# Kernel tuning notes

Hardware: AMD Instinct MI355X
Metric: run time of the kernel (lower is better)

## Reference

```python
import jax, jax.numpy as jnp
import numpy as np

N = 50000      # nodes per graph
E = 1600000    # edges per graph
D_IN = 128
D_HID = 128
D_OUT = 128
D_GF = 128
N_LAYERS = 3   # input->hid, hid->hid (hidden_layer=1), hid->out


def setup_inputs() -> dict:
    key = jax.random.key(0)
    ks = jax.random.split(key, 24)
    inp = {
        "feat_p": jax.random.normal(ks[0], (N, D_IN), jnp.float32),
        "src_p": jax.random.randint(ks[1], (E,), 0, N, jnp.int32),
        "dst_p": jax.random.randint(ks[2], (E,), 0, N, jnp.int32),
        "feat_s": jax.random.normal(ks[3], (N, D_IN), jnp.float32),
        "src_s": jax.random.randint(ks[4], (E,), 0, N, jnp.int32),
        "dst_s": jax.random.randint(ks[5], (E,), 0, N, jnp.int32),
    }
    dims = [(D_IN, D_HID), (D_HID, D_HID), (D_HID, D_OUT)]
    for i, (di, do) in enumerate(dims):
        inp[f"W{i}"] = jax.random.normal(ks[6 + 2 * i], (di, do), jnp.float32) * 0.05
        inp[f"b{i}"] = jnp.zeros((do,), jnp.float32)
    inp["Wr"] = jax.random.normal(ks[14], (D_OUT, D_GF), jnp.float32) * 0.05
    inp["br"] = jnp.zeros((D_GF,), jnp.float32)
    inp["Wm1"] = jax.random.normal(ks[15], (2 * D_GF, D_GF), jnp.float32) * 0.05
    inp["bm1"] = jnp.zeros((D_GF,), jnp.float32)
    inp["Wm2"] = jax.random.normal(ks[16], (D_GF, 1), jnp.float32) * 0.05
    inp["bm2"] = jnp.zeros((1,), jnp.float32)
    return inp


def _gcn_stack(feat, src, dst, layers):
    """Stacked GCN: mean over incoming messages, then linear.
    NOTE: the original SingleGCN never applies its ReLU (bug preserved)."""
    n = feat.shape[0]
    deg = jax.ops.segment_sum(jnp.ones_like(src, feat.dtype), dst, num_segments=n)
    inv_deg = (1.0 / jnp.maximum(deg, 1.0))[:, None]  # [N,1]
    h = feat
    for W, b in layers:
        msg = h[src]                                           # [E,d] gather
        agg = jax.ops.segment_sum(msg, dst, num_segments=n)    # [N,d] scatter-add
        h = (agg * inv_deg) @ W + b                            # mean + linear
    return h


def reference(feat_p, src_p, dst_p, feat_s, src_s, dst_s,
              W0, b0, W1, b1, W2, b2, Wr, br, Wm1, bm1, Wm2, bm2):
    layers = [(W0, b0), (W1, b1), (W2, b2)]
    h_p = _gcn_stack(feat_p, src_p, dst_p, layers)
    h_s = _gcn_stack(feat_s, src_s, dst_s, layers)
    # ReadOut: mean over nodes -> linear -> sigmoid
    g_p = jax.nn.sigmoid(jnp.mean(h_p, axis=0) @ Wr + br)  # [D_GF]
    g_s = jax.nn.sigmoid(jnp.mean(h_s, axis=0) @ Wr + br)
    # Match: concat -> linear -> linear -> sigmoid
    c = jnp.concatenate([g_p, g_s], axis=-1)               # [2*D_GF]
    d = (c @ Wm1 + bm1) @ Wm2 + bm2                        # [1]
    return jax.nn.sigmoid(d)
```

## Files before the change

### kernel.cpp

```cpp
#include <hip/hip_runtime.h>
#include <math.h>

#define D 128


__global__ __launch_bounds__(256) void scan_scatter(
        const int* __restrict__ tgt_p, const int* __restrict__ oth_p,
        const int* __restrict__ tgt_s, const int* __restrict__ oth_s,
        const float* __restrict__ w, float* __restrict__ rep,
        int E, int N, int HN, int B, int H, float scale) {
    const int b = blockIdx.x, h = blockIdx.y, g = blockIdx.z;
    const int* tgt = g ? tgt_s : tgt_p;
    const int* oth = g ? oth_s : oth_p;
    const float* wg = w ? (w + (size_t)g * N) : nullptr;

    extern __shared__ float lds[];
    {
        float4 z = make_float4(0.f, 0.f, 0.f, 0.f);
        float4* l4 = (float4*)lds;
        for (int i = threadIdx.x; i < HN / 4; i += blockDim.x) l4[i] = z;
    }
    __syncthreads();

    const int lo = h * HN;
    const int hi = min(lo + HN, N);
    const unsigned span = (unsigned)(hi - lo);
    int C = (E + B - 1) / B;
    C = (C + 15) & ~15;
    const int e0 = b * C;
    const int e1 = min(e0 + C, E);

    for (int e = e0 + (int)threadIdx.x * 16; e < e1; e += blockDim.x * 16) {
        if (e + 16 <= e1) {
            int idx[16];
            #pragma unroll
            for (int q = 0; q < 4; ++q) {
                int4 t4 = *(const int4*)(tgt + e + 4 * q);
                idx[4 * q + 0] = t4.x; idx[4 * q + 1] = t4.y;
                idx[4 * q + 2] = t4.z; idx[4 * q + 3] = t4.w;
            }
            bool hit[16];
            #pragma unroll
            for (int k = 0; k < 16; ++k) hit[k] = (unsigned)(idx[k] - lo) < span;
            if (wg) {
                int od[16];
                #pragma unroll
                for (int q = 0; q < 4; ++q) {
                    int4 o4 = *(const int4*)(oth + e + 4 * q);
                    od[4 * q + 0] = o4.x; od[4 * q + 1] = o4.y;
                    od[4 * q + 2] = o4.z; od[4 * q + 3] = o4.w;
                }
                float val[16];
                #pragma unroll
                for (int k = 0; k < 16; ++k) val[k] = hit[k] ? wg[od[k]] : 0.f;
                #pragma unroll
                for (int k = 0; k < 16; ++k)
                    if (hit[k]) atomicAdd(&lds[idx[k] - lo], val[k] * scale);
            } else {
                #pragma unroll
                for (int k = 0; k < 16; ++k)
                    if (hit[k]) atomicAdd(&lds[idx[k] - lo], 1.0f);
            }
        } else {
            for (int e2 = e; e2 < e1; ++e2) {
                int t = tgt[e2];
                if ((unsigned)(t - lo) < span) {
                    float v = wg ? wg[oth[e2]] * scale : 1.0f;
                    atomicAdd(&lds[t - lo], v);
                }
            }
        }
    }
    __syncthreads();

    float* dst = rep + (((size_t)g * H + h) * B + b) * HN;
    float4* d4 = (float4*)dst;
    const float4* l4 = (const float4*)lds;
    for (int i = threadIdx.x; i < HN / 4; i += blockDim.x) d4[i] = l4[i];
}

__global__ void reduce_inv(const float* __restrict__ rep, float* __restrict__ inv,
                           int N, int HN, int H, int B) {
    int i = (blockIdx.x * blockDim.x + threadIdx.x) * 4;
    if (i >= 2 * N) return;
    int g = (i < N) ? 0 : 1;
    int n = i - g * N;
    int h = n / HN, l = n - h * HN;
    const float* base = rep + (((size_t)g * H + h) * B) * HN + l;
    float4 s = make_float4(0.f, 0.f, 0.f, 0.f);
    #pragma unroll 16
    for (int b = 0; b < B; b++) {
        float4 v = *(const float4*)(base + (size_t)b * HN);
        s.x += v.x; s.y += v.y; s.z += v.z; s.w += v.w;
    }
    float4 r;
    r.x = 1.0f / fmaxf(s.x, 1.0f); r.y = 1.0f / fmaxf(s.y, 1.0f);
    r.z = 1.0f / fmaxf(s.z, 1.0f); r.w = 1.0f / fmaxf(s.w, 1.0f);
    *(float4*)(inv + i) = r;
}

__global__ void reduce_u(const float* __restrict__ rep, const float* __restrict__ inv,
                         float* __restrict__ out_u, float* __restrict__ out_w,
                         float* __restrict__ sums, int s_idx,
                         int N, int HN, int H, int B) {
    int i = (blockIdx.x * blockDim.x + threadIdx.x) * 4;
    float tp = 0.f, ts = 0.f;
    if (i < 2 * N) {
        int g = (i < N) ? 0 : 1;
        int n = i - g * N;
        int h = n / HN, l = n - h * HN;
        const float* base = rep + (((size_t)g * H + h) * B) * HN + l;
        float4 u = make_float4(0.f, 0.f, 0.f, 0.f);
        #pragma unroll 16
        for (int b = 0; b < B; b++) {
            float4 v = *(const float4*)(base + (size_t)b * HN);
            u.x += v.x; u.y += v.y; u.z += v.z; u.w += v.w;
        }
        if (out_u) *(float4*)(out_u + i) = u;
        if (out_w) {
            float4 iv = *(const float4*)(inv + i);
            float4 wv = make_float4(u.x * iv.x, u.y * iv.y, u.z * iv.z, u.w * iv.w);
            *(float4*)(out_w + i) = wv;
        }
        float t = u.x + u.y + u.z + u.w;
        if (g == 0) tp = t; else ts = t;
    }
    if (sums) {
        __shared__ float sm0[256], sm1[256];
        sm0[threadIdx.x] = tp;
        sm1[threadIdx.x] = ts;
        __syncthreads();
        for (int s = 128; s > 0; s >>= 1) {
            if ((int)threadIdx.x < s) {
                sm0[threadIdx.x] += sm0[threadIdx.x + s];
                sm1[threadIdx.x] += sm1[threadIdx.x + s];
            }
            __syncthreads();
        }
        if (threadIdx.x == 0) {
            if (sm0[0] != 0.f) atomicAdd(&sums[0 * 2 + s_idx], sm0[0]);
            if (sm1[0] != 0.f) atomicAdd(&sums[1 * 2 + s_idx], sm1[0]);
        }
    }
}

__global__ __launch_bounds__(256) void featsum_kernel(
        const float* __restrict__ feat_p, const float* __restrict__ feat_s,
        const float* __restrict__ u3, float* __restrict__ fpart, int N) {
    const int g = blockIdx.y;
    const float* feat = g ? feat_s : feat_p;
    const float* u = u3 + (size_t)g * N;
    const int nb = gridDim.x;
    const int col4 = threadIdx.x & 31;
    const int rgrp = threadIdx.x >> 5;
    const int rows_per_block = (N + nb - 1) / nb;
    const int r0 = blockIdx.x * rows_per_block;
    const int r1 = min(r0 + rows_per_block, N);

    const float4* f4 = (const float4*)feat;
    float4 acc = make_float4(0.f, 0.f, 0.f, 0.f);
    int n = r0 + rgrp;
    for (; n + 24 < r1; n += 32) {
        float w0 = u[n], w1 = u[n + 8], w2 = u[n + 16], w3 = u[n + 24];
        float4 v0 = f4[(size_t)n * 32 + col4];
        float4 v1 = f4[(size_t)(n + 8) * 32 + col4];
        float4 v2 = f4[(size_t)(n + 16) * 32 + col4];
        float4 v3 = f4[(size_t)(n + 24) * 32 + col4];
        acc.x += w0 * v0.x + w1 * v1.x + w2 * v2.x + w3 * v3.x;
        acc.y += w0 * v0.y + w1 * v1.y + w2 * v2.y + w3 * v3.y;
        acc.z += w0 * v0.z + w1 * v1.z + w2 * v2.z + w3 * v3.z;
        acc.w += w0 * v0.w + w1 * v1.w + w2 * v2.w + w3 * v3.w;
    }
    for (; n < r1; n += 8) {
        float wv = u[n];
        float4 v = f4[(size_t)n * 32 + col4];
        acc.x += wv * v.x; acc.y += wv * v.y; acc.z += wv * v.z; acc.w += wv * v.w;
    }
    __shared__ float4 smem[256];
    smem[threadIdx.x] = acc;
    __syncthreads();
    if (rgrp == 0) {
        float4 t = smem[col4];
        #pragma unroll
        for (int k = 1; k < 8; k++) {
            float4 o = smem[k * 32 + col4];
            t.x += o.x; t.y += o.y; t.z += o.z; t.w += o.w;
        }
        float4* dst = (float4*)(fpart + ((size_t)g * nb + blockIdx.x) * 128);
        dst[col4] = t;
    }
}

__global__ __launch_bounds__(512) void final_kernel(
        const float* __restrict__ fpart, int NB,
        const float* __restrict__ sums,
        const float* __restrict__ W0, const float* __restrict__ b0,
        const float* __restrict__ W1, const float* __restrict__ b1,
        const float* __restrict__ W2, const float* __restrict__ b2,
        const float* __restrict__ Wr, const float* __restrict__ br,
        const float* __restrict__ Wm1, const float* __restrict__ bm1,
        const float* __restrict__ Wm2, const float* __restrict__ bm2,
        float* __restrict__ out) {
    __shared__ float x[128];
    __shared__ float part[4][128];
    __shared__ float rvec[256];
    __shared__ float Avec[128], Bvec[128];
    __shared__ float gv[256];
    const int tid = threadIdx.x;
    const int j = tid & 127;
    const int h = tid >> 7;

    auto mv128 = [&](const float* __restrict__ W, float* __restrict__ buf) {
        float p = 0.f;
        const float* Wp = W + (size_t)(h * 32) * 128 + j;
        #pragma unroll
        for (int i = 0; i < 32; ++i) p += buf[h * 32 + i] * Wp[(size_t)i * 128];
        part[h][j] = p;
        __syncthreads();
        if (h == 0) buf[j] = part[0][j] + part[1][j] + part[2][j] + part[3][j];
        __syncthreads();
    };

    const int nb4 = NB / 4;
    for (int g = 0; g < 2; ++g) {
        const float* fp = fpart + (size_t)(g * NB + h * nb4) * 128 + j;
        float p = 0.f;
        #pragma unroll 16
        for (int b = 0; b < nb4; ++b) p += fp[(size_t)b * 128];
        part[h][j] = p;
        __syncthreads();
        if (h == 0) rvec[g * 128 + j] = part[0][j] + part[1][j] + part[2][j] + part[3][j];
        __syncthreads();
    }

    if (tid < 128) x[tid] = b0[tid];
    __syncthreads();
    mv128(W1, x);
    mv128(W2, x);
    if (tid < 128) Avec[tid] = x[tid];
    __syncthreads();
    if (tid < 128) x[tid] = b1[tid];
    __syncthreads();
    mv128(W2, x);
    if (tid < 128) Bvec[tid] = x[tid];
    __syncthreads();

    for (int g = 0; g < 2; ++g) {
        const float s1 = sums[g * 2 + 0];
        const float s2 = sums[g * 2 + 1];
        if (tid < 128) x[tid] = rvec[g * 128 + tid];
        __syncthreads();
        mv128(W0, x);
        mv128(W1, x);
        mv128(W2, x);
        if (tid < 128) x[tid] += s2 * Avec[tid] + s1 * Bvec[tid] + b2[tid];
        __syncthreads();
        mv128(Wr, x);
        if (tid < 128) gv[g * 128 + tid] = 1.0f / (1.0f + expf(-(x[tid] + br[tid])));
        __syncthreads();
    }

    {
        float p = 0.f;
        const float* Wp = Wm1 + (size_t)(h * 64) * 128 + j;
        #pragma unroll
        for (int i = 0; i < 64; ++i) p += gv[h * 64 + i] * Wp[(size_t)i * 128];
        part[h][j] = p;
        __syncthreads();
        if (h == 0)
            part[0][j] = (part[0][j] + part[1][j] + part[2][j] + part[3][j] + bm1[j]) * Wm2[j];
        __syncthreads();
        if (tid < 64) part[0][tid] += part[0][tid + 64];
        __syncthreads();
        if (tid < 32) part[0][tid] += part[0][tid + 32];
        __syncthreads();
        if (tid < 16) part[0][tid] += part[0][tid + 16];
        __syncthreads();
        if (tid < 8) part[0][tid] += part[0][tid + 8];
        __syncthreads();
        if (tid < 4) part[0][tid] += part[0][tid + 4];
        __syncthreads();
        if (tid < 2) part[0][tid] += part[0][tid + 2];
        __syncthreads();
        if (tid == 0) out[0] = 1.0f / (1.0f + expf(-(part[0][0] + part[0][1] + bm2[0])));
    }
}

extern "C" void kernel_launch(void* const* d_in, const int* in_sizes, int n_in,
                              void* d_out, int out_size, void* d_ws, size_t ws_size,
                              hipStream_t stream) {
    const float* feat_p = (const float*)d_in[0];
    const int*   src_p  = (const int*)d_in[1];
    const int*   dst_p  = (const int*)d_in[2];
    const float* feat_s = (const float*)d_in[3];
    const int*   src_s  = (const int*)d_in[4];
    const int*   dst_s  = (const int*)d_in[5];
    const float* W0 = (const float*)d_in[6];
    const float* b0 = (const float*)d_in[7];
    const float* W1 = (const float*)d_in[8];
    const float* b1 = (const float*)d_in[9];
    const float* W2 = (const float*)d_in[10];
    const float* b2 = (const float*)d_in[11];
    const float* Wr = (const float*)d_in[12];
    const float* br = (const float*)d_in[13];
    const float* Wm1 = (const float*)d_in[14];
    const float* bm1 = (const float*)d_in[15];
    const float* Wm2 = (const float*)d_in[16];
    const float* bm2 = (const float*)d_in[17];
    float* out = (float*)d_out;

    const int N = in_sizes[0] / D;
    const int E = in_sizes[1];
    const int N2 = 2 * N;

    const int H = 4;
    int HN = (N + H - 1) / H;
    HN = (HN + 3) & ~3;
    const int NB = 768;

    const size_t head = 16 + 4 * (size_t)N2 + (size_t)2 * NB * 128;
    size_t avail = ws_size / sizeof(float);
    int B = 8;
    if (avail > head) {
        size_t bmax = (avail - head) / ((size_t)2 * H * HN);
        if (bmax > 96) bmax = 96;
        B = (int)(bmax & ~(size_t)7);
        if (B < 1) B = 1;
    } else {
        B = 1;
    }

    float* ws    = (float*)d_ws;
    float* sums  = ws;
    float* inv   = ws + 16;
    float* w1    = inv + N2;
    float* w2    = w1 + N2;
    float* u3    = w2 + N2;
    float* fpart = u3 + N2;
    float* rep   = fpart + (size_t)2 * NB * 128;

    hipMemsetAsync(d_ws, 0, 16 * sizeof(float), stream);

    const int BT = 256;
    const dim3 sgrid(B, H, 2);
    const size_t lds_bytes = (size_t)HN * sizeof(float);
    const int gQ = (N2 / 4 + BT - 1) / BT;
    const float u0 = 1.0f / (float)N;

    scan_scatter<<<sgrid, BT, lds_bytes, stream>>>(dst_p, nullptr, dst_s, nullptr,
                                                   nullptr, rep, E, N, HN, B, H, 1.0f);
    reduce_inv<<<gQ, BT, 0, stream>>>(rep, inv, N, HN, H, B);

    scan_scatter<<<sgrid, BT, lds_bytes, stream>>>(src_p, dst_p, src_s, dst_s,
                                                   inv, rep, E, N, HN, B, H, u0);
    reduce_u<<<gQ, BT, 0, stream>>>(rep, inv, nullptr, w1, sums, 0, N, HN, H, B);

    scan_scatter<<<sgrid, BT, lds_bytes, stream>>>(src_p, dst_p, src_s, dst_s,
                                                   w1, rep, E, N, HN, B, H, 1.0f);
    reduce_u<<<gQ, BT, 0, stream>>>(rep, inv, nullptr, w2, sums, 1, N, HN, H, B);

    scan_scatter<<<sgrid, BT, lds_bytes, stream>>>(src_p, dst_p, src_s, dst_s,
                                                   w2, rep, E, N, HN, B, H, 1.0f);
    reduce_u<<<gQ, BT, 0, stream>>>(rep, inv, u3, nullptr, nullptr, 0, N, HN, H, B);

    featsum_kernel<<<dim3(NB, 2), BT, 0, stream>>>(feat_p, feat_s, u3, fpart, N);

    final_kernel<<<1, 512, 0, stream>>>(fpart, NB, sums, W0, b0, W1, b1, W2, b2,
                                        Wr, br, Wm1, bm1, Wm2, bm2, out);
}
```

Measured before the change: 311.6 us.

## Pre-bucket edges by source range so weighted scatter passes scan only matching edges

```diff
diff --git a/kernel.cpp b/kernel.cpp
--- a/kernel.cpp
+++ b/kernel.cpp
@@ -4,15 +4,11 @@
 #define D 128
 
 
-__global__ __launch_bounds__(256) void scan_scatter(
-        const int* __restrict__ tgt_p, const int* __restrict__ oth_p,
-        const int* __restrict__ tgt_s, const int* __restrict__ oth_s,
-        const float* __restrict__ w, float* __restrict__ rep,
-        int E, int N, int HN, int B, int H, float scale) {
+__global__ __launch_bounds__(256) void scan_deg(
+        const int* __restrict__ dst_p, const int* __restrict__ dst_s,
+        float* __restrict__ rep, int E, int N, int HN, int B, int H) {
     const int b = blockIdx.x, h = blockIdx.y, g = blockIdx.z;
-    const int* tgt = g ? tgt_s : tgt_p;
-    const int* oth = g ? oth_s : oth_p;
-    const float* wg = w ? (w + (size_t)g * N) : nullptr;
+    const int* tgt = g ? dst_s : dst_p;
 
     extern __shared__ float lds[];
     {
@@ -39,35 +35,13 @@
                 idx[4 * q + 0] = t4.x; idx[4 * q + 1] = t4.y;
                 idx[4 * q + 2] = t4.z; idx[4 * q + 3] = t4.w;
             }
-            bool hit[16];
-            #pragma unroll
-            for (int k = 0; k < 16; ++k) hit[k] = (unsigned)(idx[k] - lo) < span;
-            if (wg) {
-                int od[16];
-                #pragma unroll
-                for (int q = 0; q < 4; ++q) {
-                    int4 o4 = *(const int4*)(oth + e + 4 * q);
-                    od[4 * q + 0] = o4.x; od[4 * q + 1] = o4.y;
-                    od[4 * q + 2] = o4.z; od[4 * q + 3] = o4.w;
-                }
-                float val[16];
-                #pragma unroll
-                for (int k = 0; k < 16; ++k) val[k] = hit[k] ? wg[od[k]] : 0.f;
-                #pragma unroll
-                for (int k = 0; k < 16; ++k)
-                    if (hit[k]) atomicAdd(&lds[idx[k] - lo], val[k] * scale);
-            } else {
-                #pragma unroll
-                for (int k = 0; k < 16; ++k)
-                    if (hit[k]) atomicAdd(&lds[idx[k] - lo], 1.0f);
-            }
+            #pragma unroll
+            for (int k = 0; k < 16; ++k)
+                if ((unsigned)(idx[k] - lo) < span) atomicAdd(&lds[idx[k] - lo], 1.0f);
         } else {
             for (int e2 = e; e2 < e1; ++e2) {
                 int t = tgt[e2];
-                if ((unsigned)(t - lo) < span) {
-                    float v = wg ? wg[oth[e2]] * scale : 1.0f;
-                    atomicAdd(&lds[t - lo], v);
-                }
+                if ((unsigned)(t - lo) < span) atomicAdd(&lds[t - lo], 1.0f);
             }
         }
     }
@@ -79,9 +53,178 @@
     for (int i = threadIdx.x; i < HN / 4; i += blockDim.x) d4[i] = l4[i];
 }
 
-__global__ void reduce_inv(const float* __restrict__ rep, float* __restrict__ inv,
-                           int N, int HN, int H, int B) {
-    int i = (blockIdx.x * blockDim.x + threadIdx.x) * 4;
+__global__ __launch_bounds__(256) void bucket_count(
+        const int* __restrict__ src_p, const int* __restrict__ src_s,
+        int* __restrict__ cnt, float* __restrict__ sums, int E, int HN, int B0) {
+    const int b = blockIdx.x, g = blockIdx.y;
+    const int* src = g ? src_s : src_p;
+    __shared__ int c[4];
+    if (threadIdx.x < 4) c[threadIdx.x] = 0;
+    if (b == 0 && g == 0 && threadIdx.x < 16) sums[threadIdx.x] = 0.f;
+    __syncthreads();
+    int C = (E + B0 - 1) / B0; C = (C + 7) & ~7;
+    const int e0 = b * C, e1 = min(e0 + C, E);
+    const int hh = HN, h2 = 2 * HN, h3 = 3 * HN;
+    int lc0 = 0, lc1 = 0, lc2 = 0, lc3 = 0;
+    for (int e = e0 + (int)threadIdx.x * 8; e < e1; e += 2048) {
+        if (e + 8 <= e1) {
+            int4 a = *(const int4*)(src + e);
+            int4 bb = *(const int4*)(src + e + 4);
+            int v[8] = {a.x, a.y, a.z, a.w, bb.x, bb.y, bb.z, bb.w};
+            #pragma unroll
+            for (int k = 0; k < 8; ++k) {
+                int h = (v[k] >= h2) ? (v[k] >= h3 ? 3 : 2) : (v[k] >= hh ? 1 : 0);
+                lc0 += (h == 0); lc1 += (h == 1); lc2 += (h == 2); lc3 += (h == 3);
+            }
+        } else {
+            for (int e2 = e; e2 < e1; ++e2) {
+                int v = src[e2];
+                int h = (v >= h2) ? (v >= h3 ? 3 : 2) : (v >= hh ? 1 : 0);
+                lc0 += (h == 0); lc1 += (h == 1); lc2 += (h == 2); lc3 += (h == 3);
+            }
+        }
+    }
+    atomicAdd(&c[0], lc0); atomicAdd(&c[1], lc1);
+    atomicAdd(&c[2], lc2); atomicAdd(&c[3], lc3);
+    __syncthreads();
+    if (threadIdx.x < 4) cnt[((size_t)g * B0 + b) * 4 + threadIdx.x] = c[threadIdx.x];
+}
+
+__global__ __launch_bounds__(256) void bucket_prefix(
+        const int* __restrict__ cnt, int* __restrict__ base, int* __restrict__ meta,
+        int B0, int capg) {
+    __shared__ int sb[256];
+    __shared__ int tot[8], st[8];
+    const int tid = threadIdx.x;
+    for (int gh = 0; gh < 8; ++gh) {
+        int g = gh >> 2, h = gh & 3;
+        int v = cnt[((size_t)g * B0 + tid) * 4 + h];
+        sb[tid] = v;
+        __syncthreads();
+        for (int off = 1; off < 256; off <<= 1) {
+            int t = (tid >= off) ? sb[tid - off] : 0;
+            __syncthreads();
+            sb[tid] += t;
+            __syncthreads();
+        }
+        base[((size_t)g * B0 + tid) * 4 + h] = sb[tid] - v;
+        if (tid == 255) tot[gh] = sb[255];
+        __syncthreads();
+    }
+    if (tid == 0) {
+        for (int g = 0; g < 2; ++g) {
+            int off = 0;
+            for (int h = 0; h < 4; ++h) {
+                int s = (off + 3) & ~3;
+                st[g * 4 + h] = s + g * capg;
+                off = s + tot[g * 4 + h];
+            }
+        }
+    }
+    __syncthreads();
+    for (int gh = 0; gh < 8; ++gh) {
+        int g = gh >> 2, h = gh & 3;
+        base[((size_t)g * B0 + tid) * 4 + h] += st[gh];
+    }
+    if (tid < 8) { meta[tid] = st[tid]; meta[8 + tid] = tot[tid]; }
+}
+
+__global__ __launch_bounds__(256) void bucket_scatter(
+        const int* __restrict__ src_p, const int* __restrict__ dst_p,
+        const int* __restrict__ src_s, const int* __restrict__ dst_s,
+        const int* __restrict__ base, int2* __restrict__ pairs,
+        int E, int HN, int B0) {
+    const int b = blockIdx.x, g = blockIdx.y;
+    const int* src = g ? src_s : src_p;
+    const int* dst = g ? dst_s : dst_p;
+    __shared__ int cur[4];
+    if (threadIdx.x < 4) cur[threadIdx.x] = base[((size_t)g * B0 + b) * 4 + threadIdx.x];
+    __syncthreads();
+    int C = (E + B0 - 1) / B0; C = (C + 7) & ~7;
+    const int e0 = b * C, e1 = min(e0 + C, E);
+    const int hh = HN, h2 = 2 * HN, h3 = 3 * HN;
+    for (int e = e0 + (int)threadIdx.x * 8; e < e1; e += 2048) {
+        if (e + 8 <= e1) {
+            int4 sa = *(const int4*)(src + e), sb2 = *(const int4*)(src + e + 4);
+            int4 da = *(const int4*)(dst + e), db2 = *(const int4*)(dst + e + 4);
+            int sv[8] = {sa.x, sa.y, sa.z, sa.w, sb2.x, sb2.y, sb2.z, sb2.w};
+            int dv[8] = {da.x, da.y, da.z, da.w, db2.x, db2.y, db2.z, db2.w};
+            #pragma unroll
+            for (int k = 0; k < 8; ++k) {
+                int h = (sv[k] >= h2) ? (sv[k] >= h3 ? 3 : 2) : (sv[k] >= hh ? 1 : 0);
+                int pos = atomicAdd(&cur[h], 1);
+                pairs[pos] = make_int2(sv[k], dv[k]);
+            }
+        } else {
+            for (int e2 = e; e2 < e1; ++e2) {
+                int sv = src[e2], dv = dst[e2];
+                int h = (sv >= h2) ? (sv >= h3 ? 3 : 2) : (sv >= hh ? 1 : 0);
+                int pos = atomicAdd(&cur[h], 1);
+                pairs[pos] = make_int2(sv, dv);
+            }
+        }
+    }
+}
+
+__global__ __launch_bounds__(256) void scan_bucket(
+        const int2* __restrict__ pairs, const int* __restrict__ meta,
+        const float* __restrict__ w, float* __restrict__ rep,
+        int N, int HN, int B2, float scale) {
+    const int b = blockIdx.x, h = blockIdx.y, g = blockIdx.z;
+    const int start = meta[g * 4 + h];
+    const int cntgh = meta[8 + g * 4 + h];
+    const float* wg = w + (size_t)g * N;
+
+    extern __shared__ float lds[];
+    {
+        float4 z = make_float4(0.f, 0.f, 0.f, 0.f);
+        float4* l4 = (float4*)lds;
+        for (int i = threadIdx.x; i < HN / 4; i += blockDim.x) l4[i] = z;
+    }
+    __syncthreads();
+
+    const int lo = h * HN;
+    int C = (cntgh + B2 - 1) / B2; C = (C + 15) & ~15;
+    const int p0 = start + b * C;
+    const int pend = start + cntgh;
+    const int p1 = min(p0 + C, pend);
+
+    for (int p = p0 + (int)threadIdx.x * 16; p < p1; p += 4096) {
+        if (p + 16 <= p1) {
+            const int4* q = (const int4*)(pairs + p);
+            int4 qq[8];
+            #pragma unroll
+            for (int i = 0; i < 8; ++i) qq[i] = q[i];
+            int s[16], d[16];
+            #pragma unroll
+            for (int k = 0; k < 8; ++k) {
+                s[2 * k] = qq[k].x; d[2 * k] = qq[k].y;
+                s[2 * k + 1] = qq[k].z; d[2 * k + 1] = qq[k].w;
+            }
+            float v[16];
+            #pragma unroll
+            for (int k = 0; k < 16; ++k) v[k] = wg[d[k]];
+            #pragma unroll
+            for (int k = 0; k < 16; ++k) atomicAdd(&lds[s[k] - lo], v[k] * scale);
+        } else {
+            for (int p2 = p; p2 < p1; ++p2) {
+                int2 pr = pairs[p2];
+                atomicAdd(&lds[pr.x - lo], wg[pr.y] * scale);
+            }
+        }
+    }
+    __syncthreads();
+
+    float* dstp = rep + (((size_t)g * 4 + h) * B2 + b) * HN;
+    float4* d4 = (float4*)dstp;
+    const float4* l4 = (const float4*)lds;
+    for (int i = threadIdx.x; i < HN / 4; i += blockDim.x) d4[i] = l4[i];
+}
+
+__global__ __launch_bounds__(64) void reduce_inv(
+        const float* __restrict__ rep, float* __restrict__ inv,
+        int N, int HN, int H, int B) {
+    int i = (blockIdx.x * 64 + threadIdx.x) * 4;
     if (i >= 2 * N) return;
     int g = (i < N) ? 0 : 1;
     int n = i - g * N;
@@ -99,11 +242,11 @@
     *(float4*)(inv + i) = r;
 }
 
-__global__ void reduce_u(const float* __restrict__ rep, const float* __restrict__ inv,
-                         float* __restrict__ out_u, float* __restrict__ out_w,
-                         float* __restrict__ sums, int s_idx,
-                         int N, int HN, int H, int B) {
-    int i = (blockIdx.x * blockDim.x + threadIdx.x) * 4;
+__global__ __launch_bounds__(64) void reduce_u(
+        const float* __restrict__ rep, const float* __restrict__ inv,
+        float* __restrict__ out_u, float* __restrict__ out_w,
+        float* __restrict__ sums, int s_idx, int N, int HN, int H, int B) {
+    int i = (blockIdx.x * 64 + threadIdx.x) * 4;
     float tp = 0.f, ts = 0.f;
     if (i < 2 * N) {
         int g = (i < N) ? 0 : 1;
@@ -119,18 +262,16 @@
         if (out_u) *(float4*)(out_u + i) = u;
         if (out_w) {
             float4 iv = *(const float4*)(inv + i);
-            float4 wv = make_float4(u.x * iv.x, u.y * iv.y, u.z * iv.z, u.w * iv.w);
-            *(float4*)(out_w + i) = wv;
+            *(float4*)(out_w + i) = make_float4(u.x * iv.x, u.y * iv.y, u.z * iv.z, u.w * iv.w);
         }
         float t = u.x + u.y + u.z + u.w;
         if (g == 0) tp = t; else ts = t;
     }
     if (sums) {
-        __shared__ float sm0[256], sm1[256];
-        sm0[threadIdx.x] = tp;
-        sm1[threadIdx.x] = ts;
-        __syncthreads();
-        for (int s = 128; s > 0; s >>= 1) {
+        __shared__ float sm0[64], sm1[64];
+        sm0[threadIdx.x] = tp; sm1[threadIdx.x] = ts;
+        __syncthreads();
+        for (int s = 32; s > 0; s >>= 1) {
             if ((int)threadIdx.x < s) {
                 sm0[threadIdx.x] += sm0[threadIdx.x + s];
                 sm1[threadIdx.x] += sm1[threadIdx.x + s];
@@ -191,8 +332,23 @@
     }
 }
 
+__global__ __launch_bounds__(256) void fpart_reduce(
+        const float* __restrict__ fpart, float* __restrict__ fpart2, int NB) {
+    const int b = blockIdx.x, g = blockIdx.y;
+    const int j = threadIdx.x & 127, half = threadIdx.x >> 7;
+    const int per = NB / 16;
+    const float* fp = fpart + ((size_t)(g * NB + b * per + half * (per / 2))) * 128 + j;
+    float s = 0.f;
+    #pragma unroll
+    for (int k = 0; k < 24; ++k) s += fp[(size_t)k * 128];
+    __shared__ float sm[2][128];
+    sm[half][j] = s;
+    __syncthreads();
+    if (half == 0) fpart2[((size_t)g * 16 + b) * 128 + j] = sm[0][j] + sm[1][j];
+}
+
 __global__ __launch_bounds__(512) void final_kernel(
-        const float* __restrict__ fpart, int NB,
+        const float* __restrict__ fpart2,
         const float* __restrict__ sums,
         const float* __restrict__ W0, const float* __restrict__ b0,
         const float* __restrict__ W1, const float* __restrict__ b1,
@@ -221,17 +377,15 @@
         __syncthreads();
     };
 
-    const int nb4 = NB / 4;
-    for (int g = 0; g < 2; ++g) {
-        const float* fp = fpart + (size_t)(g * NB + h * nb4) * 128 + j;
-        float p = 0.f;
-        #pragma unroll 16
-        for (int b = 0; b < nb4; ++b) p += fp[(size_t)b * 128];
-        part[h][j] = p;
-        __syncthreads();
-        if (h == 0) rvec[g * 128 + j] = part[0][j] + part[1][j] + part[2][j] + part[3][j];
-        __syncthreads();
-    }
+    if (tid < 256) {
+        int g = tid >> 7;
+        const float* fp = fpart2 + (size_t)g * 2048 + (tid & 127);
+        float rv = 0.f;
+        #pragma unroll
+        for (int b = 0; b < 16; ++b) rv += fp[(size_t)b * 128];
+        rvec[tid] = rv;
+    }
+    __syncthreads();
 
     if (tid < 128) x[tid] = b0[tid];
     __syncthreads();
@@ -317,54 +471,61 @@
     int HN = (N + H - 1) / H;
     HN = (HN + 3) & ~3;
     const int NB = 768;
-
-    const size_t head = 16 + 4 * (size_t)N2 + (size_t)2 * NB * 128;
+    const int B0 = 256;
+    const int capg = E + 96;
+
+    float* ws     = (float*)d_ws;
+    float* sums   = ws;
+    float* inv    = ws + 16;
+    float* w1     = inv + N2;
+    float* w2     = w1 + N2;
+    float* u3     = w2 + N2;
+    float* fpart  = u3 + N2;
+    float* fpart2 = fpart + (size_t)2 * NB * 128;
+    int*   cnt    = (int*)(fpart2 + 2 * 16 * 128);
+    int*   base   = cnt + (size_t)2 * B0 * 4;
+    int*   meta   = base + (size_t)2 * B0 * 4;
+    size_t off_f  = (size_t)((float*)(meta + 16) - ws);
+    off_f = (off_f + 3) & ~(size_t)3;
+    int2*  pairs  = (int2*)(ws + off_f);
+    float* rep    = ws + off_f + (size_t)2 * capg * 2;
+
+    const size_t head = off_f + (size_t)2 * capg * 2;
     size_t avail = ws_size / sizeof(float);
     int B = 8;
     if (avail > head) {
         size_t bmax = (avail - head) / ((size_t)2 * H * HN);
         if (bmax > 96) bmax = 96;
         B = (int)(bmax & ~(size_t)7);
-        if (B < 1) B = 1;
-    } else {
-        B = 1;
-    }
-
-    float* ws    = (float*)d_ws;
-    float* sums  = ws;
-    float* inv   = ws + 16;
-    float* w1    = inv + N2;
-    float* w2    = w1 + N2;
-    float* u3    = w2 + N2;
-    float* fpart = u3 + N2;
-    float* rep   = fpart + (size_t)2 * NB * 128;
-
-    hipMemsetAsync(d_ws, 0, 16 * sizeof(float), stream);
+        if (B < 8) B = 8;
+    }
 
     const int BT = 256;
     const dim3 sgrid(B, H, 2);
     const size_t lds_bytes = (size_t)HN * sizeof(float);
-    const int gQ = (N2 / 4 + BT - 1) / BT;
+    const int gQ = (N2 / 4 + 63) / 64;
     const float u0 = 1.0f / (float)N;
 
-    scan_scatter<<<sgrid, BT, lds_bytes, stream>>>(dst_p, nullptr, dst_s, nullptr,
-                                                   nullptr, rep, E, N, HN, B, H, 1.0f);
-    reduce_inv<<<gQ, BT, 0, stream>>>(rep, inv, N, HN, H, B);
-
-    scan_scatter<<<sgrid, BT, lds_bytes, stream>>>(src_p, dst_p, src_s, dst_s,
-                                                   inv, rep, E, N, HN, B, H, u0);
-    reduce_u<<<gQ, BT, 0, stream>>>(rep, inv, nullptr, w1, sums, 0, N, HN, H, B);
-
-    scan_scatter<<<sgrid, BT, lds_bytes, stream>>>(src_p, dst_p, src_s, dst_s,
-                                                   w1, rep, E, N, HN, B, H, 1.0f);
-    reduce_u<<<gQ, BT, 0, stream>>>(rep, inv, nullptr, w2, sums, 1, N, HN, H, B);
-
-    scan_scatter<<<sgrid, BT, lds_bytes, stream>>>(src_p, dst_p, src_s, dst_s,
-                                                   w2, rep, E, N, HN, B, H, 1.0f);
-    reduce_u<<<gQ, BT, 0, stream>>>(rep, inv, u3, nullptr, nullptr, 0, N, HN, H, B);
+    bucket_count<<<dim3(B0, 2), BT, 0, stream>>>(src_p, src_s, cnt, sums, E, HN, B0);
+    bucket_prefix<<<1, 256, 0, stream>>>(cnt, base, meta, B0, capg);
+    bucket_scatter<<<dim3(B0, 2), BT, 0, stream>>>(src_p, dst_p, src_s, dst_s,
+                                                   base, pairs, E, HN, B0);
+
+    scan_deg<<<sgrid, BT, lds_bytes, stream>>>(dst_p, dst_s, rep, E, N, HN, B, H);
+    reduce_inv<<<gQ, 64, 0, stream>>>(rep, inv, N, HN, H, B);
+
+    scan_bucket<<<sgrid, BT, lds_bytes, stream>>>(pairs, meta, inv, rep, N, HN, B, u0);
+    reduce_u<<<gQ, 64, 0, stream>>>(rep, inv, nullptr, w1, sums, 0, N, HN, H, B);
+
+    scan_bucket<<<sgrid, BT, lds_bytes, stream>>>(pairs, meta, w1, rep, N, HN, B, 1.0f);
+    reduce_u<<<gQ, 64, 0, stream>>>(rep, inv, nullptr, w2, sums, 1, N, HN, H, B);
+
+    scan_bucket<<<sgrid, BT, lds_bytes, stream>>>(pairs, meta, w2, rep, N, HN, B, 1.0f);
+    reduce_u<<<gQ, 64, 0, stream>>>(rep, inv, u3, nullptr, nullptr, 0, N, HN, H, B);
 
     featsum_kernel<<<dim3(NB, 2), BT, 0, stream>>>(feat_p, feat_s, u3, fpart, N);
-
-    final_kernel<<<1, 512, 0, stream>>>(fpart, NB, sums, W0, b0, W1, b1, W2, b2,
+    fpart_reduce<<<dim3(16, 2), BT, 0, stream>>>(fpart, fpart2, NB);
+
+    final_kernel<<<1, 512, 0, stream>>>(fpart2, sums, W0, b0, W1, b1, W2, b2,
                                         Wr, br, Wm1, bm1, Wm2, bm2, out);
 }
```

New measurement: 351.0 us. +12.6%, slower.

## Widen scatter blocks, shrink reduce blocks, add parallel fpart pre-reduction

Applied to the files above, without the earlier changes.

```diff
diff --git a/kernel.cpp b/kernel.cpp
--- a/kernel.cpp
+++ b/kernel.cpp
@@ -4,7 +4,7 @@
 #define D 128
 
 
-__global__ __launch_bounds__(256) void scan_scatter(
+__global__ __launch_bounds__(512) void scan_scatter(
         const int* __restrict__ tgt_p, const int* __restrict__ oth_p,
         const int* __restrict__ tgt_s, const int* __restrict__ oth_s,
         const float* __restrict__ w, float* __restrict__ rep,
@@ -30,7 +30,7 @@
     const int e0 = b * C;
     const int e1 = min(e0 + C, E);
 
-    for (int e = e0 + (int)threadIdx.x * 16; e < e1; e += blockDim.x * 16) {
+    for (int e = e0 + (int)threadIdx.x * 16; e < e1; e += (int)blockDim.x * 16) {
         if (e + 16 <= e1) {
             int idx[16];
             #pragma unroll
@@ -79,9 +79,10 @@
     for (int i = threadIdx.x; i < HN / 4; i += blockDim.x) d4[i] = l4[i];
 }
 
-__global__ void reduce_inv(const float* __restrict__ rep, float* __restrict__ inv,
-                           int N, int HN, int H, int B) {
-    int i = (blockIdx.x * blockDim.x + threadIdx.x) * 4;
+__global__ __launch_bounds__(64) void reduce_inv(
+        const float* __restrict__ rep, float* __restrict__ inv,
+        int N, int HN, int H, int B) {
+    int i = (blockIdx.x * 64 + threadIdx.x) * 4;
     if (i >= 2 * N) return;
     int g = (i < N) ? 0 : 1;
     int n = i - g * N;
@@ -99,11 +100,11 @@
     *(float4*)(inv + i) = r;
 }
 
-__global__ void reduce_u(const float* __restrict__ rep, const float* __restrict__ inv,
-                         float* __restrict__ out_u, float* __restrict__ out_w,
-                         float* __restrict__ sums, int s_idx,
-                         int N, int HN, int H, int B) {
-    int i = (blockIdx.x * blockDim.x + threadIdx.x) * 4;
+__global__ __launch_bounds__(64) void reduce_u(
+        const float* __restrict__ rep, const float* __restrict__ inv,
+        float* __restrict__ out_u, float* __restrict__ out_w,
+        float* __restrict__ sums, int s_idx, int N, int HN, int H, int B) {
+    int i = (blockIdx.x * 64 + threadIdx.x) * 4;
     float tp = 0.f, ts = 0.f;
     if (i < 2 * N) {
         int g = (i < N) ? 0 : 1;
@@ -119,18 +120,16 @@
         if (out_u) *(float4*)(out_u + i) = u;
         if (out_w) {
             float4 iv = *(const float4*)(inv + i);
-            float4 wv = make_float4(u.x * iv.x, u.y * iv.y, u.z * iv.z, u.w * iv.w);
-            *(float4*)(out_w + i) = wv;
+            *(float4*)(out_w + i) = make_float4(u.x * iv.x, u.y * iv.y, u.z * iv.z, u.w * iv.w);
         }
         float t = u.x + u.y + u.z + u.w;
         if (g == 0) tp = t; else ts = t;
     }
     if (sums) {
-        __shared__ float sm0[256], sm1[256];
-        sm0[threadIdx.x] = tp;
-        sm1[threadIdx.x] = ts;
-        __syncthreads();
-        for (int s = 128; s > 0; s >>= 1) {
+        __shared__ float sm0[64], sm1[64];
+        sm0[threadIdx.x] = tp; sm1[threadIdx.x] = ts;
+        __syncthreads();
+        for (int s = 32; s > 0; s >>= 1) {
             if ((int)threadIdx.x < s) {
                 sm0[threadIdx.x] += sm0[threadIdx.x + s];
                 sm1[threadIdx.x] += sm1[threadIdx.x + s];
@@ -191,8 +190,24 @@
     }
 }
 
+__global__ __launch_bounds__(256) void fpart_reduce(
+        const float* __restrict__ fpart, float* __restrict__ fpart2, int NB) {
+    const int b = blockIdx.x, g = blockIdx.y;
+    const int j = threadIdx.x & 127, half = threadIdx.x >> 7;
+    const int per = NB / 16;
+    const int hp = per / 2;
+    const float* fp = fpart + ((size_t)(g * NB + b * per + half * hp)) * 128 + j;
+    float s = 0.f;
+    #pragma unroll 24
+    for (int k = 0; k < hp; ++k) s += fp[(size_t)k * 128];
+    __shared__ float sm[2][128];
+    sm[half][j] = s;
+    __syncthreads();
+    if (half == 0) fpart2[((size_t)g * 16 + b) * 128 + j] = sm[0][j] + sm[1][j];
+}
+
 __global__ __launch_bounds__(512) void final_kernel(
-        const float* __restrict__ fpart, int NB,
+        const float* __restrict__ fpart2,
         const float* __restrict__ sums,
         const float* __restrict__ W0, const float* __restrict__ b0,
         const float* __restrict__ W1, const float* __restrict__ b1,
@@ -221,17 +236,15 @@
         __syncthreads();
     };
 
-    const int nb4 = NB / 4;
-    for (int g = 0; g < 2; ++g) {
-        const float* fp = fpart + (size_t)(g * NB + h * nb4) * 128 + j;
-        float p = 0.f;
-        #pragma unroll 16
-        for (int b = 0; b < nb4; ++b) p += fp[(size_t)b * 128];
-        part[h][j] = p;
-        __syncthreads();
-        if (h == 0) rvec[g * 128 + j] = part[0][j] + part[1][j] + part[2][j] + part[3][j];
-        __syncthreads();
-    }
+    if (tid < 256) {
+        int g = tid >> 7;
+        const float* fp = fpart2 + (size_t)g * 2048 + (tid & 127);
+        float rv = 0.f;
+        #pragma unroll
+        for (int b = 0; b < 16; ++b) rv += fp[(size_t)b * 128];
+        rvec[tid] = rv;
+    }
+    __syncthreads();
 
     if (tid < 128) x[tid] = b0[tid];
     __syncthreads();
@@ -318,7 +331,7 @@
     HN = (HN + 3) & ~3;
     const int NB = 768;
 
-    const size_t head = 16 + 4 * (size_t)N2 + (size_t)2 * NB * 128;
+    const size_t head = 16 + 4 * (size_t)N2 + (size_t)2 * NB * 128 + 2 * 16 * 128;
     size_t avail = ws_size / sizeof(float);
     int B = 8;
     if (avail > head) {
@@ -330,41 +343,44 @@
         B = 1;
     }
 
-    float* ws    = (float*)d_ws;
-    float* sums  = ws;
-    float* inv   = ws + 16;
-    float* w1    = inv + N2;
-    float* w2    = w1 + N2;
-    float* u3    = w2 + N2;
-    float* fpart = u3 + N2;
-    float* rep   = fpart + (size_t)2 * NB * 128;
+    float* ws     = (float*)d_ws;
+    float* sums   = ws;
+    float* inv    = ws + 16;
+    float* w1     = inv + N2;
+    float* w2     = w1 + N2;
+    float* u3     = w2 + N2;
+    float* fpart  = u3 + N2;
+    float* fpart2 = fpart + (size_t)2 * NB * 128;
+    float* rep    = fpart2 + 2 * 16 * 128;
 
     hipMemsetAsync(d_ws, 0, 16 * sizeof(float), stream);
 
+    const int BTS = 512;
     const int BT = 256;
     const dim3 sgrid(B, H, 2);
     const size_t lds_bytes = (size_t)HN * sizeof(float);
-    const int gQ = (N2 / 4 + BT - 1) / BT;
+    const int gQ = (N2 / 4 + 63) / 64;
     const float u0 = 1.0f / (float)N;
 
-    scan_scatter<<<sgrid, BT, lds_bytes, stream>>>(dst_p, nullptr, dst_s, nullptr,
-                                                   nullptr, rep, E, N, HN, B, H, 1.0f);
-    reduce_inv<<<gQ, BT, 0, stream>>>(rep, inv, N, HN, H, B);
-
-    scan_scatter<<<sgrid, BT, lds_bytes, stream>>>(src_p, dst_p, src_s, dst_s,
-                                                   inv, rep, E, N, HN, B, H, u0);
-    reduce_u<<<gQ, BT, 0, stream>>>(rep, inv, nullptr, w1, sums, 0, N, HN, H, B);
-
-    scan_scatter<<<sgrid, BT, lds_bytes, stream>>>(src_p, dst_p, src_s, dst_s,
-                                                   w1, rep, E, N, HN, B, H, 1.0f);
-    reduce_u<<<gQ, BT, 0, stream>>>(rep, inv, nullptr, w2, sums, 1, N, HN, H, B);
-
-    scan_scatter<<<sgrid, BT, lds_bytes, stream>>>(src_p, dst_p, src_s, dst_s,
-                                                   w2, rep, E, N, HN, B, H, 1.0f);
-    reduce_u<<<gQ, BT, 0, stream>>>(rep, inv, u3, nullptr, nullptr, 0, N, HN, H, B);
+    scan_scatter<<<sgrid, BTS, lds_bytes, stream>>>(dst_p, nullptr, dst_s, nullptr,
+                                                    nullptr, rep, E, N, HN, B, H, 1.0f);
+    reduce_inv<<<gQ, 64, 0, stream>>>(rep, inv, N, HN, H, B);
+
+    scan_scatter<<<sgrid, BTS, lds_bytes, stream>>>(src_p, dst_p, src_s, dst_s,
+                                                    inv, rep, E, N, HN, B, H, u0);
+    reduce_u<<<gQ, 64, 0, stream>>>(rep, inv, nullptr, w1, sums, 0, N, HN, H, B);
+
+    scan_scatter<<<sgrid, BTS, lds_bytes, stream>>>(src_p, dst_p, src_s, dst_s,
+                                                    w1, rep, E, N, HN, B, H, 1.0f);
+    reduce_u<<<gQ, 64, 0, stream>>>(rep, inv, nullptr, w2, sums, 1, N, HN, H, B);
+
+    scan_scatter<<<sgrid, BTS, lds_bytes, stream>>>(src_p, dst_p, src_s, dst_s,
+                                                    w2, rep, E, N, HN, B, H, 1.0f);
+    reduce_u<<<gQ, 64, 0, stream>>>(rep, inv, u3, nullptr, nullptr, 0, N, HN, H, B);
 
     featsum_kernel<<<dim3(NB, 2), BT, 0, stream>>>(feat_p, feat_s, u3, fpart, N);
-
-    final_kernel<<<1, 512, 0, stream>>>(fpart, NB, sums, W0, b0, W1, b1, W2, b2,
+    fpart_reduce<<<dim3(16, 2), BT, 0, stream>>>(fpart, fpart2, NB);
+
+    final_kernel<<<1, 512, 0, stream>>>(fpart2, sums, W0, b0, W1, b1, W2, b2,
                                         Wr, br, Wm1, bm1, Wm2, bm2, out);
 }
```

After: 303.4 us. 2.6% less time.
